# Kernel optimization log

Measured on AMD Instinct MI355X. Metric: run time of the kernel, lower is better.

## Reference

```python
import jax, jax.numpy as jnp
import numpy as np

D, H, K, CTXW = 1024, 256, 64, 16

def _rms_norm(v, w, eps=1e-6):
    return v * jax.lax.rsqrt(jnp.mean(v * v, axis=-1, keepdims=True) + eps) * w

def setup_inputs() -> dict:
    key = jax.random.key(0)
    ks = jax.random.split(key, 20)
    s = lambda i, shape, scale=0.02: jax.random.normal(ks[i], shape, dtype=jnp.float32) * scale
    return {
        "x": jax.random.normal(ks[0], (64, 2048, D), dtype=jnp.float32),
        "context_buffer": jax.random.normal(ks[1], (1, CTXW, D), dtype=jnp.float32),
        "norm_prototypes": s(2, (K, D)),
        "ce_w1": s(3, (D, H)), "ce_b1": jnp.zeros((H,), jnp.float32),
        "ce_w2": s(4, (H, D)), "ce_b2": jnp.zeros((D,), jnp.float32),
        "rms_w": jnp.ones((D,), jnp.float32),
        "nm_w1": s(5, (3 * D, 2 * H)), "nm_b1": jnp.zeros((2 * H,), jnp.float32),
        "nm_w2": s(6, (2 * H, 1)), "nm_b2": jnp.zeros((1,), jnp.float32),
        "ns_w1": s(7, (D, H)), "ns_b1": jnp.zeros((H,), jnp.float32),
        "ns_w2": s(8, (H, K)), "ns_b2": jnp.zeros((K,), jnp.float32),
        "sv_w1": s(9, (2 * D, H)), "sv_b1": jnp.zeros((H,), jnp.float32),
        "sv_w2": s(10, (H, 1)), "sv_b2": jnp.zeros((1,), jnp.float32),
    }

def reference(x, context_buffer, norm_prototypes, ce_w1, ce_b1, ce_w2, ce_b2, rms_w,
              nm_w1, nm_b1, nm_w2, nm_b2, ns_w1, ns_b1, ns_w2, ns_b2,
              sv_w1, sv_b1, sv_w2, sv_b2, alpha=0.1):
    B = x.shape[0]
    gelu = lambda v: jax.nn.gelu(v, approximate=False)  # torch nn.GELU default (erf)
    # context encoder on mean of buffer -> [1, D], broadcast to [B, D]
    ctx = context_buffer.mean(axis=1)                          # [1, D]
    ctx_enc = _rms_norm(gelu(ctx @ ce_w1 + ce_b1) @ ce_w2 + ce_b2, rms_w)  # [1, D]
    ctx_enc = jnp.broadcast_to(ctx_enc, (B, ctx_enc.shape[-1]))            # [B, D]
    action = x.mean(axis=1)                                    # [B, D]
    # norm selector (softmax over K slots)
    norm_weights = jax.nn.softmax(gelu(ctx_enc @ ns_w1 + ns_b1) @ ns_w2 + ns_b2, axis=-1)  # [B, K]
    # norm matcher over all K slots at once; split the concat weight blocks
    wc, wa, wp = nm_w1[:1024], nm_w1[1024:2048], nm_w1[2048:]  # each [D, 2H]
    pre = (ctx_enc @ wc + action @ wa + nm_b1)[:, None, :] + (norm_prototypes @ wp)[None, :, :]  # [B,K,2H]
    conformance = jax.nn.sigmoid(jnp.squeeze(gelu(pre) @ nm_w2, -1) + nm_b2)  # [B, K]
    weighted_conf = jnp.sum(conformance * norm_weights, axis=-1)  # [B]
    violation = 1.0 - weighted_conf
    ca = jnp.concatenate([ctx_enc, action], axis=-1)            # [B, 2D]
    severity = jax.nn.sigmoid(gelu(ca @ sv_w1 + sv_b1) @ sv_w2 + sv_b2)[:, 0]  # [B]
    norm_penalty = violation * severity * alpha
    return norm_penalty, weighted_conf, violation, severity
```

## Files before the change

### kernel.cpp

```cpp
#include <hip/hip_runtime.h>
#include <math.h>

#define BD   64
#define TD   2048
#define DD   1024
#define HD   256
#define KD   64
#define CTXW 16

#define OFF_XPART  0u
#define OFF_H1P    1048576u
#define OFF_H2P    1052672u
#define OFF_CTXENC 1069056u
#define OFF_ACTION 1070080u
#define OFF_PROTOP 1135616u
#define OFF_S1P    1168384u
#define OFF_CCP    1172480u
#define OFF_AAP    1180672u
#define OFF_SVC    1442816u
#define OFF_SVA    1444864u

__device__ __forceinline__ float geluf(float v) {
    return 0.5f * v * (1.0f + erff(v * 0.70710678118654752f));
}
__device__ __forceinline__ float sigm(float v) {
    return 1.0f / (1.0f + expf(-v));
}

__global__ __launch_bounds__(256) void k1(const float* __restrict__ x,
                                          const float* __restrict__ cb,
                                          const float* __restrict__ proto,
                                          const float* __restrict__ ce_w1,
                                          const float* __restrict__ nm_w1,
                                          float* __restrict__ ws) {
    const int blk = blockIdx.x;
    const int t = threadIdx.x;
    if (blk < 1024) {
        const int b = blk >> 4, tc = blk & 15;
        const float4* xp = (const float4*)(x + (size_t)(b * TD + tc * 128) * DD);
        float4 acc = make_float4(0.f, 0.f, 0.f, 0.f);
        const float4* p = xp + t;
        #pragma unroll 4
        for (int i = 0; i < 128; ++i) {
            float4 v = p[(size_t)i * 256];
            acc.x += v.x; acc.y += v.y; acc.z += v.z; acc.w += v.w;
        }
        ((float4*)(ws + OFF_XPART + (size_t)blk * DD))[t] = acc;
    } else if (blk < 1040) {
        const int k = blk - 1024;
        __shared__ float ctxv[64];
        if (t < 64) {
            int d = k * 64 + t;
            float s = 0.f;
            #pragma unroll
            for (int w = 0; w < CTXW; ++w) s += cb[w * DD + d];
            ctxv[t] = s * (1.0f / 16.0f);
        }
        __syncthreads();
        float acc = 0.f;
        #pragma unroll 8
        for (int d = 0; d < 64; ++d)
            acc += ctxv[d] * ce_w1[(size_t)(k * 64 + d) * HD + t];
        ws[OFF_H1P + k * HD + t] = acc;
    } else {
        const int idx = blk - 1040;
        const int pg = idx >> 1, jh = idx & 1;
        __shared__ float pr[8][1024];
        for (int i = t; i < 8 * 1024; i += 256) pr[i >> 10][i & 1023] = proto[(size_t)(pg * 8) * DD + i];
        __syncthreads();
        const int j = jh * 256 + t;
        float acc[8];
        #pragma unroll
        for (int p = 0; p < 8; ++p) acc[p] = 0.f;
        for (int d = 0; d < DD; ++d) {
            float w = nm_w1[(size_t)(2048 + d) * 512 + j];
            #pragma unroll
            for (int p = 0; p < 8; ++p) acc[p] += pr[p][d] * w;
        }
        #pragma unroll
        for (int p = 0; p < 8; ++p) ws[OFF_PROTOP + (size_t)(pg * 8 + p) * 512 + j] = acc[p];
    }
}

__global__ __launch_bounds__(256) void k2(const float* __restrict__ ce_b1,
                                          const float* __restrict__ ce_w2,
                                          float* __restrict__ ws) {
    const int blk = blockIdx.x;
    const int t = threadIdx.x;
    if (blk < 16) {
        __shared__ float g1[16];
        if (t < 16) {
            int h = blk * 16 + t;
            float s = ce_b1[h];
            #pragma unroll
            for (int p = 0; p < 16; ++p) s += ws[OFF_H1P + p * HD + h];
            g1[t] = geluf(s);
        }
        __syncthreads();
        float4 acc = make_float4(0.f, 0.f, 0.f, 0.f);
        #pragma unroll
        for (int i = 0; i < 16; ++i) {
            float g = g1[i];
            float4 w = ((const float4*)(ce_w2 + (size_t)(blk * 16 + i) * DD))[t];
            acc.x += g * w.x; acc.y += g * w.y; acc.z += g * w.z; acc.w += g * w.w;
        }
        ((float4*)(ws + OFF_H2P + (size_t)blk * DD))[t] = acc;
    } else {
        const int b = blk - 16;
        float4 acc = make_float4(0.f, 0.f, 0.f, 0.f);
        #pragma unroll
        for (int k = 0; k < 16; ++k) {
            float4 v = ((const float4*)(ws + OFF_XPART + (size_t)(b * 16 + k) * DD))[t];
            acc.x += v.x; acc.y += v.y; acc.z += v.z; acc.w += v.w;
        }
        const float inv = 1.0f / 2048.0f;
        acc.x *= inv; acc.y *= inv; acc.z *= inv; acc.w *= inv;
        ((float4*)(ws + OFF_ACTION + (size_t)b * DD))[t] = acc;
    }
}

__global__ __launch_bounds__(256) void k3(const float* __restrict__ ce_b2,
                                          const float* __restrict__ rms_w,
                                          float* __restrict__ ws) {
    const int t = threadIdx.x;
    float4 acc = ((const float4*)ce_b2)[t];
    #pragma unroll
    for (int k = 0; k < 16; ++k) {
        float4 v = ((const float4*)(ws + OFF_H2P + (size_t)k * DD))[t];
        acc.x += v.x; acc.y += v.y; acc.z += v.z; acc.w += v.w;
    }
    float ss = acc.x * acc.x + acc.y * acc.y + acc.z * acc.z + acc.w * acc.w;
    __shared__ float red[4];
    __shared__ float totsh;
    const int wave = t >> 6, lane = t & 63;
    #pragma unroll
    for (int o = 32; o >= 1; o >>= 1) ss += __shfl_xor(ss, o);
    if (lane == 0) red[wave] = ss;
    __syncthreads();
    if (t == 0) totsh = red[0] + red[1] + red[2] + red[3];
    __syncthreads();
    float r = rsqrtf(totsh * (1.0f / 1024.0f) + 1e-6f);
    float4 w = ((const float4*)rms_w)[t];
    acc.x *= r * w.x; acc.y *= r * w.y; acc.z *= r * w.z; acc.w *= r * w.w;
    ((float4*)(ws + OFF_CTXENC))[t] = acc;
}

__global__ __launch_bounds__(256) void k4(const float* __restrict__ nm_w1,
                                          const float* __restrict__ ns_w1,
                                          const float* __restrict__ sv_w1,
                                          float* __restrict__ ws) {
    const int blk = blockIdx.x;
    const int t = threadIdx.x;
    if (blk < 64) {
        const int dc = blk >> 3, bg = blk & 7;
        __shared__ float al[8][128];
        for (int i = t; i < 8 * 128; i += 256) {
            int p = i >> 7, d = i & 127;
            al[p][d] = ws[OFF_ACTION + (size_t)(bg * 8 + p) * DD + dc * 128 + d];
        }
        __syncthreads();
        float acc0[8], acc1[8];
        #pragma unroll
        for (int p = 0; p < 8; ++p) { acc0[p] = 0.f; acc1[p] = 0.f; }
        for (int d = 0; d < 128; ++d) {
            const float* wrow = nm_w1 + (size_t)(1024 + dc * 128 + d) * 512;
            float w0 = wrow[t], w1 = wrow[t + 256];
            #pragma unroll
            for (int p = 0; p < 8; ++p) {
                float a = al[p][d];
                acc0[p] += a * w0; acc1[p] += a * w1;
            }
        }
        #pragma unroll
        for (int p = 0; p < 8; ++p) {
            size_t base = OFF_AAP + (size_t)(dc * 64 + bg * 8 + p) * 512;
            ws[base + t] = acc0[p];
            ws[base + t + 256] = acc1[p];
        }
    } else if (blk < 72) {
        const int dc = blk - 64;
        float acc = 0.f;
        #pragma unroll 4
        for (int d = 0; d < 128; ++d)
            acc += ws[OFF_CTXENC + dc * 128 + d] * sv_w1[(size_t)(dc * 128 + d) * HD + t];
        ws[OFF_SVC + dc * HD + t] = acc;
    } else if (blk < 136) {
        const int ii = blk - 72;
        const int dc = ii >> 3, bg = ii & 7;
        __shared__ float al[8][128];
        for (int i = t; i < 8 * 128; i += 256) {
            int p = i >> 7, d = i & 127;
            al[p][d] = ws[OFF_ACTION + (size_t)(bg * 8 + p) * DD + dc * 128 + d];
        }
        __syncthreads();
        float acc[8];
        #pragma unroll
        for (int p = 0; p < 8; ++p) acc[p] = 0.f;
        for (int d = 0; d < 128; ++d) {
            float w = sv_w1[(size_t)(1024 + dc * 128 + d) * HD + t];
            #pragma unroll
            for (int p = 0; p < 8; ++p) acc[p] += al[p][d] * w;
        }
        #pragma unroll
        for (int p = 0; p < 8; ++p)
            ws[OFF_SVA + (size_t)(dc * 64 + bg * 8 + p) * HD + t] = acc[p];
    } else if (blk < 152) {
        const int k = blk - 136;
        float acc = 0.f;
        #pragma unroll 4
        for (int d = 0; d < 64; ++d)
            acc += ws[OFF_CTXENC + k * 64 + d] * ns_w1[(size_t)(k * 64 + d) * HD + t];
        ws[OFF_S1P + k * HD + t] = acc;
    } else {
        const int k = blk - 152;
        float a0 = 0.f, a1 = 0.f;
        #pragma unroll 4
        for (int d = 0; d < 64; ++d) {
            float c = ws[OFF_CTXENC + k * 64 + d];
            const float* r = nm_w1 + (size_t)(k * 64 + d) * 512;
            a0 += c * r[t]; a1 += c * r[t + 256];
        }
        ws[OFF_CCP + k * 512 + t] = a0;
        ws[OFF_CCP + k * 512 + t + 256] = a1;
    }
}

__global__ __launch_bounds__(256) void k5(const float* __restrict__ ns_b1,
                                          const float* __restrict__ ns_w2,
                                          const float* __restrict__ ns_b2,
                                          const float* __restrict__ nm_b1,
                                          const float* __restrict__ nm_w2,
                                          const float* __restrict__ nm_b2,
                                          const float* __restrict__ sv_b1,
                                          const float* __restrict__ sv_w2,
                                          const float* __restrict__ sv_b2,
                                          const float* __restrict__ ws,
                                          float* __restrict__ out) {
    const int b = blockIdx.x;
    const int t = threadIdx.x;
    const int wave = t >> 6, lane = t & 63;
    __shared__ float g1[256];
    __shared__ float nw[64];
    __shared__ float base[512];
    __shared__ float w2s[512];
    __shared__ float conf[64];
    __shared__ float red[4];

    {
        float s = ns_b1[t];
        #pragma unroll
        for (int k = 0; k < 16; ++k) s += ws[OFF_S1P + k * HD + t];
        g1[t] = geluf(s);
    }
    __syncthreads();
    if (t < 64) {
        float s = ns_b2[t];
        for (int h = 0; h < HD; ++h) s += g1[h] * ns_w2[(size_t)h * 64 + t];
        float m = s;
        #pragma unroll
        for (int o = 32; o >= 1; o >>= 1) m = fmaxf(m, __shfl_xor(m, o));
        float e = expf(s - m);
        float tot = e;
        #pragma unroll
        for (int o = 32; o >= 1; o >>= 1) tot += __shfl_xor(tot, o);
        nw[t] = e / tot;
    }
    #pragma unroll
    for (int jj = 0; jj < 2; ++jj) {
        int j = t + jj * 256;
        float v = nm_b1[j];
        #pragma unroll
        for (int k = 0; k < 16; ++k) v += ws[OFF_CCP + k * 512 + j];
        #pragma unroll
        for (int k = 0; k < 8; ++k) v += ws[OFF_AAP + (size_t)(k * 64 + b) * 512 + j];
        base[j] = v;
        w2s[j] = nm_w2[j];
    }
    __syncthreads();
    const float b2 = nm_b2[0];
    for (int pi = 0; pi < 16; ++pi) {
        int p = wave * 16 + pi;
        const float* pp = ws + OFF_PROTOP + (size_t)p * 512;
        float s = 0.f;
        #pragma unroll
        for (int i = 0; i < 8; ++i) {
            int j = lane + 64 * i;
            s += geluf(base[j] + pp[j]) * w2s[j];
        }
        #pragma unroll
        for (int o = 32; o >= 1; o >>= 1) s += __shfl_xor(s, o);
        if (lane == 0) conf[p] = sigm(s + b2);
    }
    float sv = sv_b1[t];
    #pragma unroll
    for (int k = 0; k < 8; ++k) sv += ws[OFF_SVC + k * HD + t];
    #pragma unroll
    for (int k = 0; k < 8; ++k) sv += ws[OFF_SVA + (size_t)(k * 64 + b) * HD + t];
    float part = geluf(sv) * sv_w2[t];
    #pragma unroll
    for (int o = 32; o >= 1; o >>= 1) part += __shfl_xor(part, o);
    if (lane == 0) red[wave] = part;
    __syncthreads();
    if (t < 64) {
        float wcp = conf[t] * nw[t];
        #pragma unroll
        for (int o = 32; o >= 1; o >>= 1) wcp += __shfl_xor(wcp, o);
        if (t == 0) {
            float sev = sigm(red[0] + red[1] + red[2] + red[3] + sv_b2[0]);
            float wcf = wcp;
            float viol = 1.0f - wcf;
            out[b] = viol * sev * 0.1f;
            out[64 + b] = wcf;
            out[128 + b] = viol;
            out[192 + b] = sev;
        }
    }
}

extern "C" void kernel_launch(void* const* d_in, const int* in_sizes, int n_in,
                              void* d_out, int out_size, void* d_ws, size_t ws_size,
                              hipStream_t stream) {
    const float* x      = (const float*)d_in[0];
    const float* cb     = (const float*)d_in[1];
    const float* proto  = (const float*)d_in[2];
    const float* ce_w1  = (const float*)d_in[3];
    const float* ce_b1  = (const float*)d_in[4];
    const float* ce_w2  = (const float*)d_in[5];
    const float* ce_b2  = (const float*)d_in[6];
    const float* rms_w  = (const float*)d_in[7];
    const float* nm_w1  = (const float*)d_in[8];
    const float* nm_b1  = (const float*)d_in[9];
    const float* nm_w2  = (const float*)d_in[10];
    const float* nm_b2  = (const float*)d_in[11];
    const float* ns_w1  = (const float*)d_in[12];
    const float* ns_b1  = (const float*)d_in[13];
    const float* ns_w2  = (const float*)d_in[14];
    const float* ns_b2  = (const float*)d_in[15];
    const float* sv_w1  = (const float*)d_in[16];
    const float* sv_b1  = (const float*)d_in[17];
    const float* sv_w2  = (const float*)d_in[18];
    const float* sv_b2  = (const float*)d_in[19];
    float* ws  = (float*)d_ws;
    float* out = (float*)d_out;

    hipLaunchKernelGGL(k1, dim3(1056), dim3(256), 0, stream, x, cb, proto, ce_w1, nm_w1, ws);
    hipLaunchKernelGGL(k2, dim3(80), dim3(256), 0, stream, ce_b1, ce_w2, ws);
    hipLaunchKernelGGL(k3, dim3(1), dim3(256), 0, stream, ce_b2, rms_w, ws);
    hipLaunchKernelGGL(k4, dim3(168), dim3(256), 0, stream, nm_w1, ns_w1, sv_w1, ws);
    hipLaunchKernelGGL(k5, dim3(64), dim3(256), 0, stream,
                       ns_b1, ns_w2, ns_b2, nm_b1, nm_w2, nm_b2, sv_b1, sv_w2, sv_b2, ws, out);
}
```

Baseline: 888.2 us.

## Fuse action reduction and RMS-norm into k4, drop k3, nontemporal x loads

Removes the separate k3 launch and the action-finalization branch of k2. Each consuming block in k4 now sums the x partial sums itself, and the context blocks each recompute the context encoder's RMS norm into shared memory. k1 puts the small context and prototype blocks first and streams x with nontemporal vector loads at a higher unroll. This cuts launch count and intermediate round-trips, at the cost of redundant per-block reduction and normalization work.

```diff
diff --git a/kernel.cpp b/kernel.cpp
--- a/kernel.cpp
+++ b/kernel.cpp
@@ -11,14 +11,14 @@
 #define OFF_XPART  0u
 #define OFF_H1P    1048576u
 #define OFF_H2P    1052672u
-#define OFF_CTXENC 1069056u
-#define OFF_ACTION 1070080u
 #define OFF_PROTOP 1135616u
 #define OFF_S1P    1168384u
 #define OFF_CCP    1172480u
 #define OFF_AAP    1180672u
 #define OFF_SVC    1442816u
 #define OFF_SVA    1444864u
+
+typedef float f4 __attribute__((ext_vector_type(4)));
 
 __device__ __forceinline__ float geluf(float v) {
     return 0.5f * v * (1.0f + erff(v * 0.70710678118654752f));
@@ -35,19 +35,8 @@
                                           float* __restrict__ ws) {
     const int blk = blockIdx.x;
     const int t = threadIdx.x;
-    if (blk < 1024) {
-        const int b = blk >> 4, tc = blk & 15;
-        const float4* xp = (const float4*)(x + (size_t)(b * TD + tc * 128) * DD);
-        float4 acc = make_float4(0.f, 0.f, 0.f, 0.f);
-        const float4* p = xp + t;
-        #pragma unroll 4
-        for (int i = 0; i < 128; ++i) {
-            float4 v = p[(size_t)i * 256];
-            acc.x += v.x; acc.y += v.y; acc.z += v.z; acc.w += v.w;
-        }
-        ((float4*)(ws + OFF_XPART + (size_t)blk * DD))[t] = acc;
-    } else if (blk < 1040) {
-        const int k = blk - 1024;
+    if (blk < 16) {
+        const int k = blk;
         __shared__ float ctxv[64];
         if (t < 64) {
             int d = k * 64 + t;
@@ -62,8 +51,8 @@
         for (int d = 0; d < 64; ++d)
             acc += ctxv[d] * ce_w1[(size_t)(k * 64 + d) * HD + t];
         ws[OFF_H1P + k * HD + t] = acc;
-    } else {
-        const int idx = blk - 1040;
+    } else if (blk < 32) {
+        const int idx = blk - 16;
         const int pg = idx >> 1, jh = idx & 1;
         __shared__ float pr[8][1024];
         for (int i = t; i < 8 * 1024; i += 256) pr[i >> 10][i & 1023] = proto[(size_t)(pg * 8) * DD + i];
@@ -72,6 +61,7 @@
         float acc[8];
         #pragma unroll
         for (int p = 0; p < 8; ++p) acc[p] = 0.f;
+        #pragma unroll 4
         for (int d = 0; d < DD; ++d) {
             float w = nm_w1[(size_t)(2048 + d) * 512 + j];
             #pragma unroll
@@ -79,6 +69,17 @@
         }
         #pragma unroll
         for (int p = 0; p < 8; ++p) ws[OFF_PROTOP + (size_t)(pg * 8 + p) * 512 + j] = acc[p];
+    } else {
+        const int xb = blk - 32;
+        const int b = xb >> 4, tc = xb & 15;
+        const f4* p = (const f4*)(x + (size_t)(b * TD + tc * 128) * DD) + t;
+        f4 acc = {0.f, 0.f, 0.f, 0.f};
+        #pragma unroll 8
+        for (int i = 0; i < 128; ++i) {
+            f4 v = __builtin_nontemporal_load(p + (size_t)i * 256);
+            acc += v;
+        }
+        ((f4*)(ws + OFF_XPART + (size_t)xb * DD))[t] = acc;
     }
 }
 
@@ -87,141 +88,132 @@
                                           float* __restrict__ ws) {
     const int blk = blockIdx.x;
     const int t = threadIdx.x;
-    if (blk < 16) {
-        __shared__ float g1[16];
-        if (t < 16) {
-            int h = blk * 16 + t;
-            float s = ce_b1[h];
-            #pragma unroll
-            for (int p = 0; p < 16; ++p) s += ws[OFF_H1P + p * HD + h];
-            g1[t] = geluf(s);
-        }
-        __syncthreads();
-        float4 acc = make_float4(0.f, 0.f, 0.f, 0.f);
-        #pragma unroll
-        for (int i = 0; i < 16; ++i) {
-            float g = g1[i];
-            float4 w = ((const float4*)(ce_w2 + (size_t)(blk * 16 + i) * DD))[t];
-            acc.x += g * w.x; acc.y += g * w.y; acc.z += g * w.z; acc.w += g * w.w;
-        }
-        ((float4*)(ws + OFF_H2P + (size_t)blk * DD))[t] = acc;
-    } else {
-        const int b = blk - 16;
-        float4 acc = make_float4(0.f, 0.f, 0.f, 0.f);
-        #pragma unroll
-        for (int k = 0; k < 16; ++k) {
-            float4 v = ((const float4*)(ws + OFF_XPART + (size_t)(b * 16 + k) * DD))[t];
-            acc.x += v.x; acc.y += v.y; acc.z += v.z; acc.w += v.w;
-        }
-        const float inv = 1.0f / 2048.0f;
-        acc.x *= inv; acc.y *= inv; acc.z *= inv; acc.w *= inv;
-        ((float4*)(ws + OFF_ACTION + (size_t)b * DD))[t] = acc;
-    }
-}
-
-__global__ __launch_bounds__(256) void k3(const float* __restrict__ ce_b2,
-                                          const float* __restrict__ rms_w,
-                                          float* __restrict__ ws) {
-    const int t = threadIdx.x;
-    float4 acc = ((const float4*)ce_b2)[t];
-    #pragma unroll
-    for (int k = 0; k < 16; ++k) {
-        float4 v = ((const float4*)(ws + OFF_H2P + (size_t)k * DD))[t];
-        acc.x += v.x; acc.y += v.y; acc.z += v.z; acc.w += v.w;
-    }
-    float ss = acc.x * acc.x + acc.y * acc.y + acc.z * acc.z + acc.w * acc.w;
-    __shared__ float red[4];
-    __shared__ float totsh;
-    const int wave = t >> 6, lane = t & 63;
-    #pragma unroll
-    for (int o = 32; o >= 1; o >>= 1) ss += __shfl_xor(ss, o);
-    if (lane == 0) red[wave] = ss;
+    __shared__ float g1[16];
+    if (t < 16) {
+        int h = blk * 16 + t;
+        float s = ce_b1[h];
+        #pragma unroll
+        for (int p = 0; p < 16; ++p) s += ws[OFF_H1P + p * HD + h];
+        g1[t] = geluf(s);
+    }
     __syncthreads();
-    if (t == 0) totsh = red[0] + red[1] + red[2] + red[3];
-    __syncthreads();
-    float r = rsqrtf(totsh * (1.0f / 1024.0f) + 1e-6f);
-    float4 w = ((const float4*)rms_w)[t];
-    acc.x *= r * w.x; acc.y *= r * w.y; acc.z *= r * w.z; acc.w *= r * w.w;
-    ((float4*)(ws + OFF_CTXENC))[t] = acc;
+    float4 acc = make_float4(0.f, 0.f, 0.f, 0.f);
+    #pragma unroll
+    for (int i = 0; i < 16; ++i) {
+        float g = g1[i];
+        float4 w = ((const float4*)(ce_w2 + (size_t)(blk * 16 + i) * DD))[t];
+        acc.x += g * w.x; acc.y += g * w.y; acc.z += g * w.z; acc.w += g * w.w;
+    }
+    ((float4*)(ws + OFF_H2P + (size_t)blk * DD))[t] = acc;
 }
 
 __global__ __launch_bounds__(256) void k4(const float* __restrict__ nm_w1,
                                           const float* __restrict__ ns_w1,
                                           const float* __restrict__ sv_w1,
+                                          const float* __restrict__ ce_b2,
+                                          const float* __restrict__ rms_w,
                                           float* __restrict__ ws) {
     const int blk = blockIdx.x;
     const int t = threadIdx.x;
-    if (blk < 64) {
-        const int dc = blk >> 3, bg = blk & 7;
-        __shared__ float al[8][128];
-        for (int i = t; i < 8 * 128; i += 256) {
+    __shared__ float al[8][128];
+    __shared__ float ce[1024];
+    __shared__ float red[4];
+    __shared__ float totsh;
+
+    if (blk < 128) {
+        const int ii = (blk < 64) ? blk : (blk - 64);
+        const int dc = ii >> 3, bg = ii & 7;
+        for (int i = t; i < 1024; i += 256) {
             int p = i >> 7, d = i & 127;
-            al[p][d] = ws[OFF_ACTION + (size_t)(bg * 8 + p) * DD + dc * 128 + d];
-        }
-        __syncthreads();
-        float acc0[8], acc1[8];
-        #pragma unroll
-        for (int p = 0; p < 8; ++p) { acc0[p] = 0.f; acc1[p] = 0.f; }
-        for (int d = 0; d < 128; ++d) {
-            const float* wrow = nm_w1 + (size_t)(1024 + dc * 128 + d) * 512;
-            float w0 = wrow[t], w1 = wrow[t + 256];
+            int row = (bg * 8 + p) * 16;
+            float s = 0.f;
+            #pragma unroll
+            for (int k = 0; k < 16; ++k)
+                s += ws[OFF_XPART + (size_t)(row + k) * DD + dc * 128 + d];
+            al[p][d] = s * (1.0f / 2048.0f);
+        }
+        __syncthreads();
+        if (blk < 64) {
+            float acc0[8], acc1[8];
+            #pragma unroll
+            for (int p = 0; p < 8; ++p) { acc0[p] = 0.f; acc1[p] = 0.f; }
+            for (int d = 0; d < 128; ++d) {
+                const float* wrow = nm_w1 + (size_t)(1024 + dc * 128 + d) * 512;
+                float w0 = wrow[t], w1 = wrow[t + 256];
+                #pragma unroll
+                for (int p = 0; p < 8; ++p) {
+                    float a = al[p][d];
+                    acc0[p] += a * w0; acc1[p] += a * w1;
+                }
+            }
             #pragma unroll
             for (int p = 0; p < 8; ++p) {
-                float a = al[p][d];
-                acc0[p] += a * w0; acc1[p] += a * w1;
+                size_t base = OFF_AAP + (size_t)(dc * 64 + bg * 8 + p) * 512;
+                ws[base + t] = acc0[p];
+                ws[base + t + 256] = acc1[p];
             }
-        }
-        #pragma unroll
-        for (int p = 0; p < 8; ++p) {
-            size_t base = OFF_AAP + (size_t)(dc * 64 + bg * 8 + p) * 512;
-            ws[base + t] = acc0[p];
-            ws[base + t + 256] = acc1[p];
-        }
-    } else if (blk < 72) {
-        const int dc = blk - 64;
-        float acc = 0.f;
-        #pragma unroll 4
-        for (int d = 0; d < 128; ++d)
-            acc += ws[OFF_CTXENC + dc * 128 + d] * sv_w1[(size_t)(dc * 128 + d) * HD + t];
-        ws[OFF_SVC + dc * HD + t] = acc;
-    } else if (blk < 136) {
-        const int ii = blk - 72;
-        const int dc = ii >> 3, bg = ii & 7;
-        __shared__ float al[8][128];
-        for (int i = t; i < 8 * 128; i += 256) {
-            int p = i >> 7, d = i & 127;
-            al[p][d] = ws[OFF_ACTION + (size_t)(bg * 8 + p) * DD + dc * 128 + d];
-        }
-        __syncthreads();
-        float acc[8];
-        #pragma unroll
-        for (int p = 0; p < 8; ++p) acc[p] = 0.f;
-        for (int d = 0; d < 128; ++d) {
-            float w = sv_w1[(size_t)(1024 + dc * 128 + d) * HD + t];
-            #pragma unroll
-            for (int p = 0; p < 8; ++p) acc[p] += al[p][d] * w;
-        }
-        #pragma unroll
-        for (int p = 0; p < 8; ++p)
-            ws[OFF_SVA + (size_t)(dc * 64 + bg * 8 + p) * HD + t] = acc[p];
-    } else if (blk < 152) {
-        const int k = blk - 136;
-        float acc = 0.f;
-        #pragma unroll 4
-        for (int d = 0; d < 64; ++d)
-            acc += ws[OFF_CTXENC + k * 64 + d] * ns_w1[(size_t)(k * 64 + d) * HD + t];
-        ws[OFF_S1P + k * HD + t] = acc;
+        } else {
+            float acc[8];
+            #pragma unroll
+            for (int p = 0; p < 8; ++p) acc[p] = 0.f;
+            for (int d = 0; d < 128; ++d) {
+                float w = sv_w1[(size_t)(1024 + dc * 128 + d) * HD + t];
+                #pragma unroll
+                for (int p = 0; p < 8; ++p) acc[p] += al[p][d] * w;
+            }
+            #pragma unroll
+            for (int p = 0; p < 8; ++p)
+                ws[OFF_SVA + (size_t)(dc * 64 + bg * 8 + p) * HD + t] = acc[p];
+        }
     } else {
-        const int k = blk - 152;
-        float a0 = 0.f, a1 = 0.f;
-        #pragma unroll 4
-        for (int d = 0; d < 64; ++d) {
-            float c = ws[OFF_CTXENC + k * 64 + d];
-            const float* r = nm_w1 + (size_t)(k * 64 + d) * 512;
-            a0 += c * r[t]; a1 += c * r[t + 256];
-        }
-        ws[OFF_CCP + k * 512 + t] = a0;
-        ws[OFF_CCP + k * 512 + t + 256] = a1;
+        float4 acc = ((const float4*)ce_b2)[t];
+        #pragma unroll
+        for (int k = 0; k < 16; ++k) {
+            float4 v = ((const float4*)(ws + OFF_H2P + (size_t)k * DD))[t];
+            acc.x += v.x; acc.y += v.y; acc.z += v.z; acc.w += v.w;
+        }
+        float ss = acc.x * acc.x + acc.y * acc.y + acc.z * acc.z + acc.w * acc.w;
+        const int wave = t >> 6, lane = t & 63;
+        #pragma unroll
+        for (int o = 32; o >= 1; o >>= 1) ss += __shfl_xor(ss, o);
+        if (lane == 0) red[wave] = ss;
+        __syncthreads();
+        if (t == 0) totsh = red[0] + red[1] + red[2] + red[3];
+        __syncthreads();
+        float r = rsqrtf(totsh * (1.0f / 1024.0f) + 1e-6f);
+        float4 w = ((const float4*)rms_w)[t];
+        ce[4 * t + 0] = acc.x * r * w.x;
+        ce[4 * t + 1] = acc.y * r * w.y;
+        ce[4 * t + 2] = acc.z * r * w.z;
+        ce[4 * t + 3] = acc.w * r * w.w;
+        __syncthreads();
+
+        if (blk < 136) {
+            const int dc = blk - 128;
+            float a = 0.f;
+            #pragma unroll 4
+            for (int d = 0; d < 128; ++d)
+                a += ce[dc * 128 + d] * sv_w1[(size_t)(dc * 128 + d) * HD + t];
+            ws[OFF_SVC + dc * HD + t] = a;
+        } else if (blk < 152) {
+            const int k = blk - 136;
+            float a = 0.f;
+            #pragma unroll 4
+            for (int d = 0; d < 64; ++d)
+                a += ce[k * 64 + d] * ns_w1[(size_t)(k * 64 + d) * HD + t];
+            ws[OFF_S1P + k * HD + t] = a;
+        } else {
+            const int k = blk - 152;
+            float a0 = 0.f, a1 = 0.f;
+            #pragma unroll 4
+            for (int d = 0; d < 64; ++d) {
+                float c = ce[k * 64 + d];
+                const float* r2 = nm_w1 + (size_t)(k * 64 + d) * 512;
+                a0 += c * r2[t]; a1 += c * r2[t + 256];
+            }
+            ws[OFF_CCP + k * 512 + t] = a0;
+            ws[OFF_CCP + k * 512 + t + 256] = a1;
+        }
     }
 }
 
@@ -344,9 +336,8 @@
     float* out = (float*)d_out;
 
     hipLaunchKernelGGL(k1, dim3(1056), dim3(256), 0, stream, x, cb, proto, ce_w1, nm_w1, ws);
-    hipLaunchKernelGGL(k2, dim3(80), dim3(256), 0, stream, ce_b1, ce_w2, ws);
-    hipLaunchKernelGGL(k3, dim3(1), dim3(256), 0, stream, ce_b2, rms_w, ws);
-    hipLaunchKernelGGL(k4, dim3(168), dim3(256), 0, stream, nm_w1, ns_w1, sv_w1, ws);
+    hipLaunchKernelGGL(k2, dim3(16), dim3(256), 0, stream, ce_b1, ce_w2, ws);
+    hipLaunchKernelGGL(k4, dim3(168), dim3(256), 0, stream, nm_w1, ns_w1, sv_w1, ce_b2, rms_w, ws);
     hipLaunchKernelGGL(k5, dim3(64), dim3(256), 0, stream,
                        ns_b1, ns_w2, ns_b2, nm_b1, nm_w2, nm_b2, sv_b1, sv_w2, sv_b2, ws, out);
 }
```

Measured after the change: 845.9 us. 4.8% less time.
